# Optimization experiments

Hardware: AMD Instinct MI355X
Metric: run time of the kernel (lower is better)

Reference implementation:

```python
import jax, jax.numpy as jnp
import numpy as np

B, L, IN = 4, 2048, 64
D, N, K, NL, NC = 256, 16, 32, 2, 2


def _ln(x, g, b):
    m = x.mean(-1, keepdims=True)
    v = ((x - m) ** 2).mean(-1, keepdims=True)
    return (x - m) * jax.lax.rsqrt(v + 1e-5) * g + b


def _dwconv(x, w, b):
    # depthwise conv1d, kernel 3, padding 1; x: [B,L,D], w: [D,3]
    xp = jnp.pad(x, ((0, 0), (1, 1), (0, 0)))
    return xp[:, :-2] * w[:, 0] + xp[:, 1:-1] * w[:, 1] + xp[:, 2:] * w[:, 2] + b


def _ssm(x, loglam, wd, bd, wb, wc, wo, bo):
    # x: [B,L,D]
    lam = jax.nn.softplus(loglam)                      # [D,N]
    delta = jax.nn.softplus(x @ wd + bd)[..., None]    # [B,L,D,1]
    Bt = (x @ wb)[:, :, None, :]                       # [B,L,1,N]
    Ct = (x @ wc)[:, :, None, :]                       # [B,L,1,N]
    A_d = jnp.exp(-delta * lam)                        # [B,L,D,N]
    B_d = delta * Bt                                   # [B,L,D,N]
    A_l = jnp.moveaxis(A_d, 1, 0)                      # [L,B,D,N]
    B_l = jnp.moveaxis(B_d, 1, 0)

    def step(h, ab):
        a, b = ab
        h = a * h + b
        return h, h

    h0 = jnp.zeros((x.shape[0], D, N), x.dtype)
    _, hs = jax.lax.scan(step, h0, (A_l, B_l))         # [L,B,D,N]
    ys = hs * jnp.moveaxis(Ct, 1, 0)                   # [L,B,D,N]
    out = jnp.moveaxis(ys, 0, 1).reshape(x.shape[0], x.shape[1], D * N)
    return out @ wo + bo


def _temporal_block(x, lg, lb, cw, cb, loglam, wd, bd, wb, wc, wo, bo, gw, gb, pw, pb):
    res = x
    xn = _ln(x, lg, lb)
    xc = _dwconv(xn, cw, cb)
    xs = _ssm(xc, loglam, wd, bd, wb, wc, wo, bo)
    g = jax.nn.sigmoid(xn @ gw + gb)
    return (xs * g) @ pw + pb + res


def _spectral(x, fr, fi):
    X = jnp.fft.rfft(x, axis=1)                        # [B,F,D] complex64
    mag = jnp.abs(X).mean(axis=(0, 2))                 # [F]
    k = min(K, X.shape[1])
    _, idx = jax.lax.top_k(mag, k)
    filt = (fr[:, :k] + 1j * fi[:, :k]).T              # [k,D]
    Xk = X[:, idx, :] * filt[None]
    Xo = jnp.zeros(X.shape, X.dtype).at[:, idx, :].set(Xk)
    return jnp.fft.irfft(Xo, n=x.shape[1], axis=1)


def setup_inputs() -> dict:
    key = jax.random.key(0)
    ks = jax.random.split(key, 32)
    rn = lambda i, shape, s=0.02: jax.random.normal(ks[i], shape, jnp.float32) * s
    inp = {
        "x": jax.random.normal(ks[0], (B, L, IN), jnp.float32),
        "w_in": rn(1, (IN, D), 0.1), "b_in": jnp.zeros((D,), jnp.float32),
        "ln_g": jnp.ones((NL, D), jnp.float32), "ln_b": jnp.zeros((NL, D), jnp.float32),
        "conv_w": rn(2, (NL, D, 3), 0.3), "conv_b": jnp.zeros((NL, D), jnp.float32),
        "loglam": jax.random.uniform(ks[3], (NL, D, N), jnp.float32),
        "wd": rn(4, (NL, D, D), 0.05), "bd": jnp.zeros((NL, D), jnp.float32),
        "wb": rn(5, (NL, D, N), 0.05), "wc": rn(6, (NL, D, N), 0.05),
        "wo": rn(7, (NL, D * N, D), 0.01), "bo": jnp.zeros((NL, D), jnp.float32),
        "gate_w": rn(8, (NL, D, D), 0.05), "gate_b": jnp.zeros((NL, D), jnp.float32),
        "proj_w": rn(9, (NL, D, D), 0.05), "proj_b": jnp.zeros((NL, D), jnp.float32),
        "fr": rn(10, (D, K)), "fi": rn(11, (D, K)),
        "alpha": jnp.full((D,), 0.5, jnp.float32), "beta": jnp.full((D,), 0.5, jnp.float32),
        "g_out": jnp.ones((D,), jnp.float32), "b_out": jnp.zeros((D,), jnp.float32),
        "hw1": rn(12, (D, D // 2), 0.05), "hb1": jnp.zeros((D // 2,), jnp.float32),
        "hw2": rn(13, (D // 2, NC), 0.05), "hb2": jnp.zeros((NC,), jnp.float32),
    }
    return inp


def reference(x, w_in, b_in, ln_g, ln_b, conv_w, conv_b, loglam, wd, bd, wb, wc, wo, bo,
              gate_w, gate_b, proj_w, proj_b, fr, fi, alpha, beta, g_out, b_out,
              hw1, hb1, hw2, hb2):
    h = x @ w_in + b_in                                # [B,L,D]
    xt = h
    for i in range(NL):
        xt = _temporal_block(xt, ln_g[i], ln_b[i], conv_w[i], conv_b[i], loglam[i],
                             wd[i], bd[i], wb[i], wc[i], wo[i], bo[i],
                             gate_w[i], gate_b[i], proj_w[i], proj_b[i])
    xs = _spectral(h, fr, fi)
    z = alpha * xt + beta * xs
    z = _ln(z, g_out, b_out)
    zl = z[:, -1, :]                                   # [B,D]
    hid = jax.nn.silu(zl @ hw1 + hb1)                  # dropout is identity in eval
    return hid @ hw2 + hb2                             # [B,NC]
```

## Files before the change

### kernel.cpp

```cpp
#include <hip/hip_runtime.h>
#include <hip/hip_bf16.h>
#include <math.h>

#define BB   4
#define LL   2048
#define INF_ 64
#define DD   256
#define NN   16
#define KK   32
#define BLn  (BB*LL)
#define FCNT 1025
#define FSTR 1056
#define SKM  8192
#define SKN  256
#define PSZ  ((size_t)SKM * SKN)
#define IX(x) ((x) + ((x) >> 6))

typedef short short4v __attribute__((ext_vector_type(4)));
typedef short short8 __attribute__((ext_vector_type(8)));
typedef float f32x4  __attribute__((ext_vector_type(4)));

__device__ __forceinline__ float softplusf(float x) {
    return x > 20.f ? x : log1pf(__expf(x));
}
__device__ __forceinline__ float sigmoidf_(float x) {
    return 1.f / (1.f + __expf(-x));
}
__device__ __forceinline__ short bfs(float v) {
    __hip_bfloat16 h = __float2bfloat16(v);
    return *reinterpret_cast<short*>(&h);
}

__global__ void prep_kernel(const float* __restrict__ wd, const float* __restrict__ gw,
                            const float* __restrict__ pw, const float* __restrict__ wo,
                            const float* __restrict__ wb, const float* __restrict__ wc,
                            const float* __restrict__ w_in, float* __restrict__ tab,
                            __hip_bfloat16* __restrict__ cat0, __hip_bfloat16* __restrict__ cat1,
                            __hip_bfloat16* __restrict__ gwt, __hip_bfloat16* __restrict__ pwt,
                            __hip_bfloat16* __restrict__ wot, __hip_bfloat16* __restrict__ wint) {
    __shared__ float t[32][33];
    const int tid = threadIdx.x;
    int blk = blockIdx.x;
    if (blk < 8) {
        int i = blk * 256 + tid;
        if (i < 2048) {
            double ang = 2.0 * 3.14159265358979323846 * (double)i / 2048.0;
            tab[i]        = (float)cos(ang);
            tab[2048 + i] = (float)sin(ang);
        }
        return;
    }
    blk -= 8;
    const float* W; __hip_bfloat16* Wt; int K, N, bx, by;
    if (blk < 64)        { W = wd;                     Wt = cat0; K = 256;  N = 256; bx = blk & 7; by = blk >> 3; }
    else if (blk < 128)  { int q = blk - 64;  W = wd + 65536; Wt = cat1; K = 256; N = 256; bx = q & 7; by = q >> 3; }
    else if (blk < 192)  { int q = blk - 128; W = gw;  Wt = gwt;  K = 256;  N = 256; bx = q & 7; by = q >> 3; }
    else if (blk < 256)  { int q = blk - 192; W = pw;  Wt = pwt;  K = 256;  N = 256; bx = q & 7; by = q >> 3; }
    else if (blk < 1280) { int q = blk - 256; W = wo;  Wt = wot;  K = 4096; N = 256; bx = q & 7; by = q >> 3; }
    else if (blk < 1344) {
        int j = (blk - 1280) & 31;
        const float* src0 = (blk < 1312) ? wb : wb + DD * NN;
        const float* src1 = (blk < 1312) ? wc : wc + DD * NN;
        __hip_bfloat16* cat = (blk < 1312) ? cat0 : cat1;
        const float* src = (j < 16) ? src0 : src1;
        cat[(size_t)(256 + j) * 256 + tid] = __float2bfloat16(src[tid * 16 + (j & 15)]);
        return;
    } else { int q = blk - 1344; W = w_in; Wt = wint; K = 64; N = 256; bx = q & 7; by = q >> 3; }
    const int k0 = by * 32, n0 = bx * 32;
    if (k0 >= K) return;
    const int tx = tid & 31, ty = tid >> 5;
    for (int r = ty; r < 32; r += 8) t[r][tx] = W[(size_t)(k0 + r) * N + n0 + tx];
    __syncthreads();
    for (int r = ty; r < 32; r += 8)
        Wt[(size_t)(n0 + r) * K + k0 + tx] = __float2bfloat16(t[tx][r]);
}

__global__ __launch_bounds__(256)
void gemm_in_kernel(const float* __restrict__ x, const __hip_bfloat16* __restrict__ wint,
                    const float* __restrict__ b_in, float* __restrict__ h,
                    float* __restrict__ ht) {
    __shared__ alignas(16) short As[64][72];
    __shared__ alignas(16) short Bs[64][72];
    __shared__ float ts[64][68];
    const int tid = threadIdx.x;
    const int w = tid >> 6, lane = tid & 63;
    const int hi = lane >> 4, lo = lane & 15;
    const int row0 = blockIdx.y * 64, col0 = blockIdx.x * 64;
    const short* B = (const short*)wint;
#pragma unroll
    for (int e = 0; e < 4; ++e) {
        int q = e * 256 + tid;
        int r = q >> 4, c4 = (q & 15) * 4;
        float4 v = *(const float4*)&x[(size_t)(row0 + r) * 64 + c4];
        short4v s = {bfs(v.x), bfs(v.y), bfs(v.z), bfs(v.w)};
        *(short4v*)&As[r][c4] = s;
    }
#pragma unroll
    for (int e = 0; e < 2; ++e) {
        int q = e * 256 + tid;
        int r = q >> 3, c8 = (q & 7) * 8;
        *(short8*)&Bs[r][c8] = *(const short8*)&B[(size_t)(col0 + r) * 64 + c8];
    }
    __syncthreads();
    f32x4 acc[4];
    f32x4 zz = {0.f, 0.f, 0.f, 0.f};
#pragma unroll
    for (int n = 0; n < 4; ++n) acc[n] = zz;
#pragma unroll
    for (int s = 0; s < 2; ++s) {
        short8 af = *(const short8*)&As[w * 16 + lo][s * 32 + hi * 8];
#pragma unroll
        for (int n = 0; n < 4; ++n) {
            short8 bf = *(const short8*)&Bs[n * 16 + lo][s * 32 + hi * 8];
            acc[n] = __builtin_amdgcn_mfma_f32_16x16x32_bf16(af, bf, acc[n], 0, 0, 0);
        }
    }
#pragma unroll
    for (int n = 0; n < 4; ++n)
#pragma unroll
        for (int r = 0; r < 4; ++r) {
            const int row = row0 + w * 16 + hi * 4 + r;
            const int col = col0 + n * 16 + lo;
            float v = acc[n][r] + b_in[col];
            h[(size_t)row * 256 + col] = v;
            ts[n * 16 + lo][w * 16 + hi * 4 + r] = v;
        }
    __syncthreads();
    const int b = row0 >> 11, l0 = row0 & 2047, d0 = col0;
    const int dr = tid >> 2, seg = tid & 3;
    float* dst = ht + ((size_t)(b * 256 + d0 + dr)) * LL + l0 + seg * 16;
#pragma unroll
    for (int j = 0; j < 4; ++j)
        *(f32x4*)&dst[j * 4] = *(const f32x4*)&ts[dr][seg * 16 + j * 4];
}

__global__ __launch_bounds__(256)
void lnconv_kernel(const float* __restrict__ X, const float* __restrict__ g,
                   const float* __restrict__ bln, const float* __restrict__ cw,
                   const float* __restrict__ cb, __hip_bfloat16* __restrict__ xn_bf,
                   __hip_bfloat16* __restrict__ xc_bf) {
    __shared__ float xs[34][260];
    const int tid = threadIdx.x;
    const int w = tid >> 6, lane = tid & 63;
    const int blk = blockIdx.x;
    const int b = (blk * 32) >> 11, L0 = (blk * 32) & 2047;
    const float4 g4 = *(const float4*)&g[lane * 4];
    const float4 b4 = *(const float4*)&bln[lane * 4];
    for (int slot = w; slot < 34; slot += 4) {
        const int l = L0 - 1 + slot;
        if (l < 0 || l >= LL) {
            f32x4 z = {0.f, 0.f, 0.f, 0.f};
            *(f32x4*)&xs[slot][lane * 4] = z;
            continue;
        }
        float4 v = *(const float4*)&X[((size_t)b * LL + l) * DD + lane * 4];
        float s = v.x + v.y + v.z + v.w;
#pragma unroll
        for (int off = 1; off < 64; off <<= 1) s += __shfl_xor(s, off);
        float m = s * (1.f / DD);
        float cx = v.x - m, cy = v.y - m, cz = v.z - m, cw_ = v.w - m;
        float q = cx * cx + cy * cy + cz * cz + cw_ * cw_;
#pragma unroll
        for (int off = 1; off < 64; off <<= 1) q += __shfl_xor(q, off);
        float inv = rsqrtf(q * (1.f / DD) + 1e-5f);
        f32x4 y;
        y[0] = cx * inv * g4.x + b4.x;
        y[1] = cy * inv * g4.y + b4.y;
        y[2] = cz * inv * g4.z + b4.z;
        y[3] = cw_ * inv * g4.w + b4.w;
        *(f32x4*)&xs[slot][lane * 4] = y;
        if (slot >= 1 && slot <= 32) {
            short4v s4 = {bfs(y[0]), bfs(y[1]), bfs(y[2]), bfs(y[3])};
            *(short4v*)&xn_bf[((size_t)b * LL + l) * DD + lane * 4] = s4;
        }
    }
    __syncthreads();
    const int d = tid;
    const float w0 = cw[d * 3 + 0], w1 = cw[d * 3 + 1], w2 = cw[d * 3 + 2], cbd = cb[d];
    float xm = xs[0][d], x0 = xs[1][d];
    for (int rw = 0; rw < 32; ++rw) {
        float xp = xs[rw + 2][d];
        xc_bf[((size_t)b * LL + L0 + rw) * DD + d] =
            __float2bfloat16(fmaf(w0, xm, fmaf(w1, x0, fmaf(w2, xp, cbd))));
        xm = x0; x0 = xp;
    }
}

template<int MODE>
__global__ __launch_bounds__(256)
void gemm_core(const short* __restrict__ A, const short* __restrict__ Bw,
               const float* __restrict__ bias, const float* __restrict__ x1,
               const float* __restrict__ x2, float* __restrict__ o0,
               float* __restrict__ o1, float* __restrict__ o2,
               __hip_bfloat16* __restrict__ ob) {
    __shared__ alignas(16) short As[2][64][40];
    __shared__ alignas(16) short Bs[2][64][40];
    const int tid = threadIdx.x;
    const int w = tid >> 6, lane = tid & 63;
    const int hi = lane >> 4, lo = lane & 15;
    const int row0 = blockIdx.y * 64, col0 = blockIdx.x * 64;
    f32x4 acc[4];
    f32x4 zz = {0.f, 0.f, 0.f, 0.f};
#pragma unroll
    for (int n = 0; n < 4; ++n) acc[n] = zz;
    const int sr = tid >> 2, sc = (tid & 3) * 8;
    short8 pa = *(const short8*)&A[(size_t)(row0 + sr) * 256 + sc];
    short8 pb = *(const short8*)&Bw[(size_t)(col0 + sr) * 256 + sc];
    *(short8*)&As[0][sr][sc] = pa;
    *(short8*)&Bs[0][sr][sc] = pb;
    pa = *(const short8*)&A[(size_t)(row0 + sr) * 256 + 32 + sc];
    pb = *(const short8*)&Bw[(size_t)(col0 + sr) * 256 + 32 + sc];
    __syncthreads();
    int cur = 0;
    for (int it = 0; it < 8; ++it) {
        if (it + 1 < 8) {
            *(short8*)&As[cur ^ 1][sr][sc] = pa;
            *(short8*)&Bs[cur ^ 1][sr][sc] = pb;
        }
        if (it + 2 < 8) {
            const int k0 = (it + 2) << 5;
            pa = *(const short8*)&A[(size_t)(row0 + sr) * 256 + k0 + sc];
            pb = *(const short8*)&Bw[(size_t)(col0 + sr) * 256 + k0 + sc];
        }
        short8 af = *(const short8*)&As[cur][w * 16 + lo][hi * 8];
        short8 bfr[4];
#pragma unroll
        for (int n = 0; n < 4; ++n)
            bfr[n] = *(const short8*)&Bs[cur][n * 16 + lo][hi * 8];
#pragma unroll
        for (int n = 0; n < 4; ++n)
            acc[n] = __builtin_amdgcn_mfma_f32_16x16x32_bf16(af, bfr[n], acc[n], 0, 0, 0);
        __syncthreads();
        cur ^= 1;
    }
#pragma unroll
    for (int n = 0; n < 4; ++n) {
#pragma unroll
        for (int r = 0; r < 4; ++r) {
            const int row = row0 + w * 16 + hi * 4 + r;
            const int col = col0 + n * 16 + lo;
            float v = acc[n][r];
            if constexpr (MODE == 0) {
                if (col < 256)      o0[(size_t)row * 256 + col] = softplusf(v + bias[col]);
                else if (col < 272) o1[(size_t)row * 16 + col - 256] = v;
                else if (col < 288) o2[(size_t)row * 16 + col - 272] = v;
            } else if constexpr (MODE == 1) {
                float gv = sigmoidf_(v + bias[col]);
                size_t idx = (size_t)row * 256 + col;
                float s = x1[idx] + x1[PSZ + idx] + x2[col];
                ob[idx] = __float2bfloat16(gv * s);
            } else {
                o0[(size_t)row * 256 + col] = v + bias[col] + x1[(size_t)row * 256 + col];
            }
        }
    }
}

__global__ __launch_bounds__(256)
void gemm_sk_kernel(const __hip_bfloat16* __restrict__ Abf, const __hip_bfloat16* __restrict__ Wt,
                    float* __restrict__ P) {
    __shared__ alignas(16) short As[2][64][40];
    __shared__ alignas(16) short Bs[2][64][40];
    const int tid = threadIdx.x;
    const int f = blockIdx.x;
    const int xcd = f & 7, s = f >> 3;
    const int col = s & 3, u = s >> 2;
    const int rowkb = xcd + u * 8;
    const int row = rowkb & 127, kb = rowkb >> 7;
    const int row0 = row * 64, col0 = col * 64;
    const size_t kbase = (size_t)kb * 2048;
    const int w = tid >> 6, lane = tid & 63;
    const int hi = lane >> 4, lo = lane & 15;
    const short* A = (const short*)Abf;
    const short* B = (const short*)Wt;
    f32x4 acc[4];
    f32x4 zz = {0.f, 0.f, 0.f, 0.f};
#pragma unroll
    for (int n = 0; n < 4; ++n) acc[n] = zz;
    const int sr = tid >> 2, sc = (tid & 3) * 8;
    short8 pa = *(const short8*)&A[(size_t)(row0 + sr) * 4096 + kbase + sc];
    short8 pb = *(const short8*)&B[(size_t)(col0 + sr) * 4096 + kbase + sc];
    *(short8*)&As[0][sr][sc] = pa;
    *(short8*)&Bs[0][sr][sc] = pb;
    pa = *(const short8*)&A[(size_t)(row0 + sr) * 4096 + kbase + 32 + sc];
    pb = *(const short8*)&B[(size_t)(col0 + sr) * 4096 + kbase + 32 + sc];
    __syncthreads();
    int cur = 0;
    for (int it = 0; it < 64; ++it) {
        if (it + 1 < 64) {
            *(short8*)&As[cur ^ 1][sr][sc] = pa;
            *(short8*)&Bs[cur ^ 1][sr][sc] = pb;
        }
        if (it + 2 < 64) {
            const size_t k0 = kbase + ((it + 2) << 5);
            pa = *(const short8*)&A[(size_t)(row0 + sr) * 4096 + k0 + sc];
            pb = *(const short8*)&B[(size_t)(col0 + sr) * 4096 + k0 + sc];
        }
        short8 af = *(const short8*)&As[cur][w * 16 + lo][hi * 8];
        short8 bfr[4];
#pragma unroll
        for (int n = 0; n < 4; ++n)
            bfr[n] = *(const short8*)&Bs[cur][n * 16 + lo][hi * 8];
#pragma unroll
        for (int n = 0; n < 4; ++n)
            acc[n] = __builtin_amdgcn_mfma_f32_16x16x32_bf16(af, bfr[n], acc[n], 0, 0, 0);
        __syncthreads();
        cur ^= 1;
    }
    float* Pk = P + (size_t)kb * PSZ;
#pragma unroll
    for (int n = 0; n < 4; ++n)
#pragma unroll
        for (int r = 0; r < 4; ++r) {
            int rr = row0 + w * 16 + hi * 4 + r;
            int cc = col0 + n * 16 + lo;
            Pk[(size_t)rr * SKN + cc] = acc[n][r];
        }
}

template<int PHASE>
__global__ void ssm_chunk_kernel(const float* __restrict__ delta, const float* __restrict__ Bt,
                                 const float* __restrict__ Ct, const float* __restrict__ loglam,
                                 float* __restrict__ sA, float* __restrict__ sB,
                                 __hip_bfloat16* __restrict__ ys) {
    __shared__ float dl[128][16];
    __shared__ float btl[128][16];
    __shared__ float ctl[128][16];
    const int dblk = blockIdx.x, c = blockIdx.y, b = blockIdx.z;
    const int tid = threadIdx.x;
    const size_t lbase = (size_t)b * LL + c * 128;
    for (int i = tid; i < 2048; i += 256) {
        int l = i >> 4, q = i & 15;
        dl[l][q]  = delta[(lbase + l) * DD + dblk * 16 + q];
        btl[l][q] = Bt[(lbase + l) * NN + q];
        if (PHASE == 1) ctl[l][q] = Ct[(lbase + l) * NN + q];
    }
    float hv = 0.f, ap = 1.f;
    if (PHASE == 1) {
        for (int cc = 0; cc < c; ++cc) {
            size_t oi = ((size_t)(b * 16 + cc)) * 4096 + dblk * 256 + tid;
            hv = fmaf(sA[oi], hv, sB[oi]);
        }
    }
    __syncthreads();
    const int dloc = tid >> 4, n = tid & 15;
    const float lam = softplusf(loglam[(dblk * 16 + dloc) * NN + n]);
    for (int l = 0; l < 128; ++l) {
        float dv = dl[l][dloc];
        float a = __expf(-dv * lam);
        hv = fmaf(a, hv, dv * btl[l][n]);
        if (PHASE == 0) ap *= a;
        else ys[(lbase + l) * (DD * NN) + dblk * 256 + tid] = __float2bfloat16(hv * ctl[l][n]);
    }
    if (PHASE == 0) {
        size_t oi = ((size_t)(b * 16 + c)) * 4096 + dblk * 256 + tid;
        sA[oi] = ap; sB[oi] = hv;
    }
}

__global__ void last_ssm_part_kernel(const float* __restrict__ sA, const float* __restrict__ sB,
                                     const float* __restrict__ Ct,
                                     const float* __restrict__ wo, float* __restrict__ part) {
    __shared__ float hC[4][128];
    const int c = blockIdx.x, tid = threadIdx.x;
    const int p0 = c * 128;
#pragma unroll
    for (int e = 0; e < 2; ++e) {
        int i = e * 256 + tid;
        int b = i >> 7, p = i & 127;
        float hh = 0.f;
#pragma unroll
        for (int cc = 0; cc < 16; ++cc) {
            size_t oi = ((size_t)(b * 16 + cc)) * 4096 + p0 + p;
            hh = fmaf(sA[oi], hh, sB[oi]);
        }
        hC[b][p] = hh * Ct[((size_t)b * LL + (LL - 1)) * NN + (p & 15)];
    }
    __syncthreads();
    float a0 = 0.f, a1 = 0.f, a2 = 0.f, a3 = 0.f;
    for (int p = 0; p < 128; ++p) {
        float wv = wo[(size_t)(p0 + p) * DD + tid];
        a0 = fmaf(hC[0][p], wv, a0);
        a1 = fmaf(hC[1][p], wv, a1);
        a2 = fmaf(hC[2][p], wv, a2);
        a3 = fmaf(hC[3][p], wv, a3);
    }
    part[(0 * 32 + c) * DD + tid] = a0;
    part[(1 * 32 + c) * DD + tid] = a1;
    part[(2 * 32 + c) * DD + tid] = a2;
    part[(3 * 32 + c) * DD + tid] = a3;
}

__global__ void last_redproj_kernel(const float* __restrict__ part, const float* __restrict__ bo,
                                    const __hip_bfloat16* __restrict__ xn, const float* __restrict__ gw,
                                    const float* __restrict__ gb, const float* __restrict__ pw,
                                    const float* __restrict__ pb, const float* __restrict__ resid,
                                    float* __restrict__ xtlast) {
    __shared__ float xrow[256];
    __shared__ float xsg[256];
    const int b = blockIdx.x, d = threadIdx.x;
    float ol = bo[d];
#pragma unroll
    for (int c = 0; c < 32; ++c) ol += part[(b * 32 + c) * DD + d];
    const size_t rbase = ((size_t)b * LL + (LL - 1)) * DD;
    xrow[d] = __bfloat162float(xn[rbase + d]);
    __syncthreads();
    float acc = gb[d];
    for (int k = 0; k < 256; ++k) acc = fmaf(xrow[k], gw[(size_t)k * DD + d], acc);
    xsg[d] = ol * sigmoidf_(acc);
    __syncthreads();
    float acc2 = pb[d];
    for (int k = 0; k < 256; ++k) acc2 = fmaf(xsg[k], pw[(size_t)k * DD + d], acc2);
    xtlast[b * DD + d] = acc2 + resid[rbase + d];
}

__global__ __launch_bounds__(256)
void fft2_kernel(const float* __restrict__ ht, const float* __restrict__ tab,
                 float* __restrict__ Xre, float* __restrict__ Xim) {
    __shared__ float re[2080];
    __shared__ float im[2080];
    __shared__ float c2[2048];
    __shared__ float s2[2048];
    const int tid = threadIdx.x;
    const int pair = blockIdx.x;
    const int b = pair >> 7, d0 = pair & 127;
    for (int p = tid; p < 2048; p += 256) {
        if (p >= 1) {
            int lh = 31 - __clz((unsigned)p);
            int j = p - (1 << lh);
            int t = j << (10 - lh);
            c2[p] = tab[t]; s2[p] = tab[2048 + t];
        }
    }
    const float* ha = ht + ((size_t)b * 256 + d0) * LL;
    const float* hb = ha + (size_t)128 * LL;
    for (int i = tid; i < 2048; i += 256) {
        int r = (int)(__brev((unsigned)i) >> 21);
        re[IX(r)] = ha[i];
        im[IX(r)] = hb[i];
    }
    __syncthreads();
#pragma unroll
    for (int s = 1; s <= 11; ++s) {
        const int half = 1 << (s - 1);
#pragma unroll
        for (int e = 0; e < 4; ++e) {
            int q = e * 256 + tid;
            int j = q & (half - 1);
            int i0 = ((q >> (s - 1)) << s) + j;
            int i1 = i0 + half;
            float wr = c2[half + j], wi = -s2[half + j];
            float xr = re[IX(i1)], xi = im[IX(i1)];
            float tr = xr * wr - xi * wi;
            float ti = xr * wi + xi * wr;
            float ur = re[IX(i0)], ui = im[IX(i0)];
            re[IX(i0)] = ur + tr; im[IX(i0)] = ui + ti;
            re[IX(i1)] = ur - tr; im[IX(i1)] = ui - ti;
        }
        __syncthreads();
    }
    const int seqa = b * 256 + d0;
    float* xra = Xre + (size_t)seqa * FSTR;
    float* xia = Xim + (size_t)seqa * FSTR;
    float* xrb = xra + (size_t)128 * FSTR;
    float* xib = xia + (size_t)128 * FSTR;
    for (int f = tid; f < FCNT; f += 256) {
        int nf = (2048 - f) & 2047;
        float zrf = re[IX(f)], zif = im[IX(f)];
        float zrn = re[IX(nf)], zin = im[IX(nf)];
        xra[f] = 0.5f * (zrf + zrn);
        xia[f] = 0.5f * (zif - zin);
        xrb[f] = 0.5f * (zif + zin);
        xib[f] = 0.5f * (zrn - zrf);
    }
}

__global__ void mag_part_kernel(const float* __restrict__ Xre, const float* __restrict__ Xim,
                                float* __restrict__ part) {
    const int fb = blockIdx.x, sb = blockIdx.y;
    const int tid = threadIdx.x;
    const int f = fb * 256 + tid;
    float s = 0.f;
    if (f < FCNT) {
        for (int q = 0; q < 64; ++q) {
            size_t base = (size_t)(sb * 64 + q) * FSTR + f;
            float re = Xre[base], im = Xim[base];
            s += sqrtf(re * re + im * im);
        }
    }
    part[sb * 1280 + fb * 256 + tid] = s;
}

__global__ void topk_kernel(const float* __restrict__ part, int* __restrict__ sel) {
    __shared__ float vals[1280];
    __shared__ float wval[4][32];
    __shared__ int   widx[4][32];
    const int tid = threadIdx.x;
    const int lane = tid & 63, wid = tid >> 6;
    for (int i = tid; i < 1280; i += 256) {
        float v = -1e30f;
        if (i < FCNT) {
            v = 0.f;
#pragma unroll
            for (int sb = 0; sb < 16; ++sb) v += part[sb * 1280 + i];
        }
        vals[i] = v;
    }
    __syncthreads();
    const int base = wid * 320;
    for (int k = 0; k < 32; ++k) {
        float bv = -1e30f; int bi = 0x7fffffff;
#pragma unroll
        for (int q = 0; q < 5; ++q) {
            int i = base + q * 64 + lane;
            float v = vals[i];
            if (v > bv) { bv = v; bi = i; }
        }
#pragma unroll
        for (int off = 32; off > 0; off >>= 1) {
            float ov = __shfl_down(bv, off);
            int   oi = __shfl_down(bi, off);
            if (ov > bv || (ov == bv && oi < bi)) { bv = ov; bi = oi; }
        }
        bv = __shfl(bv, 0);
        bi = __shfl(bi, 0);
        if (lane == 0) { wval[wid][k] = bv; widx[wid][k] = bi; }
        vals[bi] = -1e30f;
    }
    __syncthreads();
    if (tid == 0) {
        int p0 = 0, p1 = 0, p2 = 0, p3 = 0;
        for (int k = 0; k < 32; ++k) {
            float v0 = wval[0][p0], v1 = wval[1][p1], v2 = wval[2][p2], v3 = wval[3][p3];
            int bw = 0; float bv = v0;
            if (v1 > bv) { bv = v1; bw = 1; }
            if (v2 > bv) { bv = v2; bw = 2; }
            if (v3 > bv) { bv = v3; bw = 3; }
            if (bw == 0)      { sel[k] = widx[0][p0++]; }
            else if (bw == 1) { sel[k] = widx[1][p1++]; }
            else if (bw == 2) { sel[k] = widx[2][p2++]; }
            else              { sel[k] = widx[3][p3++]; }
        }
    }
}

__global__ void head_kernel(const float* __restrict__ Xre, const float* __restrict__ Xim,
                            const int* __restrict__ sel, const float* __restrict__ fr,
                            const float* __restrict__ fi, const float* __restrict__ tab,
                            const float* __restrict__ xtlast,
                            const float* __restrict__ alpha, const float* __restrict__ beta,
                            const float* __restrict__ gout, const float* __restrict__ bout,
                            const float* __restrict__ hw1, const float* __restrict__ hb1,
                            const float* __restrict__ hw2, const float* __restrict__ hb2,
                            float* __restrict__ out) {
    __shared__ float red[256];
    __shared__ float z[256];
    __shared__ float hid[128];
    const int b = blockIdx.x, tid = threadIdx.x;
    const size_t sbase = (size_t)(b * 256 + tid) * FSTR;
    float xsl = 0.f;
    for (int j = 0; j < 32; ++j) {
        int f = sel[j];
        float xr = Xre[sbase + f];
        float xi = Xim[sbase + f];
        float frv = fr[tid * KK + j], fiv = fi[tid * KK + j];
        float xor_ = xr * frv - xi * fiv;
        float xoi  = xr * fiv + xi * frv;
        int kk2 = (f * (LL - 1)) & (LL - 1);
        float c = tab[kk2], s = tab[2048 + kk2];
        float w = (f == 0 || f == 1024) ? 1.f : 2.f;
        xsl = fmaf(w, xor_ * c - xoi * s, xsl);
    }
    xsl *= (1.f / LL);
    float zv = alpha[tid] * xtlast[b * 256 + tid] + beta[tid] * xsl;
    red[tid] = zv; __syncthreads();
    for (int s = 128; s > 0; s >>= 1) { if (tid < s) red[tid] += red[tid + s]; __syncthreads(); }
    float m = red[0] * (1.f / DD);
    __syncthreads();
    float c = zv - m;
    red[tid] = c * c; __syncthreads();
    for (int s = 128; s > 0; s >>= 1) { if (tid < s) red[tid] += red[tid + s]; __syncthreads(); }
    float var = red[0] * (1.f / DD);
    z[tid] = c * rsqrtf(var + 1e-5f) * gout[tid] + bout[tid];
    __syncthreads();
    if (tid < 128) {
        float a = hb1[tid];
        for (int k = 0; k < 256; ++k) a = fmaf(z[k], hw1[(size_t)k * 128 + tid], a);
        hid[tid] = a * sigmoidf_(a);
    }
    __syncthreads();
    if (tid < 2) {
        float a = hb2[tid];
        for (int k = 0; k < 128; ++k) a = fmaf(hid[k], hw2[(size_t)k * 2 + tid], a);
        out[b * 2 + tid] = a;
    }
}

extern "C" void kernel_launch(void* const* d_in, const int* in_sizes, int n_in,
                              void* d_out, int out_size, void* d_ws, size_t ws_size,
                              hipStream_t stream) {
    const float* x      = (const float*)d_in[0];
    const float* w_in   = (const float*)d_in[1];
    const float* b_in   = (const float*)d_in[2];
    const float* ln_g   = (const float*)d_in[3];
    const float* ln_b   = (const float*)d_in[4];
    const float* conv_w = (const float*)d_in[5];
    const float* conv_b = (const float*)d_in[6];
    const float* loglam = (const float*)d_in[7];
    const float* wd     = (const float*)d_in[8];
    const float* bd     = (const float*)d_in[9];
    const float* wb     = (const float*)d_in[10];
    const float* wc     = (const float*)d_in[11];
    const float* wo     = (const float*)d_in[12];
    const float* bo     = (const float*)d_in[13];
    const float* gw     = (const float*)d_in[14];
    const float* gb     = (const float*)d_in[15];
    const float* pw     = (const float*)d_in[16];
    const float* pb     = (const float*)d_in[17];
    const float* fr     = (const float*)d_in[18];
    const float* fi     = (const float*)d_in[19];
    const float* alpha  = (const float*)d_in[20];
    const float* beta   = (const float*)d_in[21];
    const float* gout   = (const float*)d_in[22];
    const float* bout   = (const float*)d_in[23];
    const float* hw1    = (const float*)d_in[24];
    const float* hb1    = (const float*)d_in[25];
    const float* hw2    = (const float*)d_in[26];
    const float* hb2    = (const float*)d_in[27];

    float* ws = (float*)d_ws;
    size_t o = 0;
    auto alloc = [&](size_t n) { float* p = ws + o; o += (n + 15) & ~(size_t)15; return p; };

    const size_t BLnDD = (size_t)BLn * DD;
    float* h      = alloc(BLnDD);
    float* xt1    = alloc(BLnDD);
    float* ht     = alloc(BLnDD);
    float* delta  = alloc(BLnDD);
    float* Pbuf   = alloc(2 * PSZ);
    float* Btm    = alloc((size_t)BLn * NN);
    float* Ctm    = alloc((size_t)BLn * NN);
    float* tab    = alloc(4096);
    float* ysf    = alloc(BLnDD * NN / 2);
    float* sA     = alloc((size_t)BB * 16 * 4096);
    float* sB     = alloc((size_t)BB * 16 * 4096);
    float* xnbf_f = alloc(BLnDD / 2);
    float* xcbf_f = alloc(BLnDD / 2);
    float* xsgf   = alloc(BLnDD / 2);
    float* cat0_f = alloc((size_t)320 * 256 / 2);
    float* cat1_f = alloc((size_t)320 * 256 / 2);
    float* gwt_f  = alloc((size_t)DD * DD / 2);
    float* pwt_f  = alloc((size_t)DD * DD / 2);
    float* wot_f  = alloc((size_t)DD * NN * DD / 2);
    float* wint_f = alloc((size_t)DD * 64 / 2);
    float* magp   = alloc(16 * 1280);
    int*   sel    = (int*)alloc(32);
    float* lpart  = alloc((size_t)BB * 32 * DD);
    float* xtlast = alloc(BB * DD);

    __hip_bfloat16* ys    = (__hip_bfloat16*)ysf;
    float*          Xre   = ysf;
    float*          Xim   = ysf + (size_t)1024 * FSTR;
    __hip_bfloat16* xn_bf = (__hip_bfloat16*)xnbf_f;
    __hip_bfloat16* xc_bf = (__hip_bfloat16*)xcbf_f;
    __hip_bfloat16* xsg_bf= (__hip_bfloat16*)xsgf;
    __hip_bfloat16* cat0  = (__hip_bfloat16*)cat0_f;
    __hip_bfloat16* cat1  = (__hip_bfloat16*)cat1_f;
    __hip_bfloat16* gwt   = (__hip_bfloat16*)gwt_f;
    __hip_bfloat16* pwt   = (__hip_bfloat16*)pwt_f;
    __hip_bfloat16* wot   = (__hip_bfloat16*)wot_f;
    __hip_bfloat16* wint  = (__hip_bfloat16*)wint_f;

    const dim3 blk(256);

    prep_kernel<<<1368, blk, 0, stream>>>(wd, gw, pw, wo, wb, wc, w_in, tab,
                                          cat0, cat1, gwt, pwt, wot, wint);
    gemm_in_kernel<<<dim3(4, 128), blk, 0, stream>>>(x, wint, b_in, h, ht);

    const dim3 qgrid(5, BLn / 64);
    const dim3 ggrid(4, BLn / 64);
    const dim3 sgrid(16, 16, BB);

    lnconv_kernel<<<BLn / 32, blk, 0, stream>>>(h, ln_g, ln_b, conv_w, conv_b, xn_bf, xc_bf);
    gemm_core<0><<<qgrid, blk, 0, stream>>>((const short*)xc_bf, (const short*)cat0,
                                            bd, nullptr, nullptr, delta, Btm, Ctm, nullptr);
    ssm_chunk_kernel<0><<<sgrid, blk, 0, stream>>>(delta, Btm, nullptr, loglam,
                                                   sA, sB, nullptr);
    ssm_chunk_kernel<1><<<sgrid, blk, 0, stream>>>(delta, Btm, Ctm, loglam,
                                                   sA, sB, ys);
    gemm_sk_kernel<<<1024, blk, 0, stream>>>(ys, wot, Pbuf);
    gemm_core<1><<<ggrid, blk, 0, stream>>>((const short*)xn_bf, (const short*)gwt,
                                            gb, Pbuf, bo, nullptr, nullptr, nullptr, xsg_bf);
    gemm_core<2><<<ggrid, blk, 0, stream>>>((const short*)xsg_bf, (const short*)pwt,
                                            pb, h, nullptr, xt1, nullptr, nullptr, nullptr);

    lnconv_kernel<<<BLn / 32, blk, 0, stream>>>(xt1, ln_g + DD, ln_b + DD,
                                                conv_w + DD * 3, conv_b + DD, xn_bf, xc_bf);
    gemm_core<0><<<qgrid, blk, 0, stream>>>((const short*)xc_bf, (const short*)cat1,
                                            bd + DD, nullptr, nullptr, delta, Btm, Ctm, nullptr);
    ssm_chunk_kernel<0><<<sgrid, blk, 0, stream>>>(delta, Btm, nullptr, loglam + DD * NN,
                                                   sA, sB, nullptr);
    last_ssm_part_kernel<<<32, blk, 0, stream>>>(sA, sB, Ctm, wo + (size_t)DD * NN * DD, lpart);
    last_redproj_kernel<<<BB, blk, 0, stream>>>(lpart, bo + DD, xn_bf,
                                                gw + (size_t)DD * DD, gb + DD,
                                                pw + (size_t)DD * DD, pb + DD, xt1, xtlast);

    fft2_kernel<<<512, blk, 0, stream>>>(ht, tab, Xre, Xim);
    mag_part_kernel<<<dim3(5, 16), blk, 0, stream>>>(Xre, Xim, magp);
    topk_kernel<<<1, blk, 0, stream>>>(magp, sel);

    head_kernel<<<BB, blk, 0, stream>>>(Xre, Xim, sel, fr, fi, tab, xtlast,
                                        alpha, beta, gout, bout,
                                        hw1, hb1, hw2, hb2, (float*)d_out);
}
```

Measured before the change: 280.2 us.

## Enlarge split-K GEMM tile to 128 rows and restructure double-buffered pipeline

The split-K output-projection GEMM now computes 128x64 tiles per block, with each wave doing two M sub-tiles, so every B fragment loaded from shared memory feeds two MFMAs. This halves the block count and cuts B-operand reloads. Both GEMM kernels also get a manually unrolled two-stage register/LDS pipeline that uses a raw barrier with an lgkmcnt wait instead of __syncthreads. The changes add register and LDS pressure, and with fewer blocks there may be less parallelism to hide latency.

```diff
diff --git a/kernel.cpp b/kernel.cpp
--- a/kernel.cpp
+++ b/kernel.cpp
@@ -30,6 +30,8 @@
     __hip_bfloat16 h = __float2bfloat16(v);
     return *reinterpret_cast<short*>(&h);
 }
+#define RAWBAR() do { asm volatile("s_waitcnt lgkmcnt(0)" ::: "memory"); \
+                      __builtin_amdgcn_s_barrier(); } while (0)
 
 __global__ void prep_kernel(const float* __restrict__ wd, const float* __restrict__ gw,
                             const float* __restrict__ pw, const float* __restrict__ wo,
@@ -204,34 +206,38 @@
 #pragma unroll
     for (int n = 0; n < 4; ++n) acc[n] = zz;
     const int sr = tid >> 2, sc = (tid & 3) * 8;
-    short8 pa = *(const short8*)&A[(size_t)(row0 + sr) * 256 + sc];
-    short8 pb = *(const short8*)&Bw[(size_t)(col0 + sr) * 256 + sc];
-    *(short8*)&As[0][sr][sc] = pa;
-    *(short8*)&Bs[0][sr][sc] = pb;
-    pa = *(const short8*)&A[(size_t)(row0 + sr) * 256 + 32 + sc];
-    pb = *(const short8*)&Bw[(size_t)(col0 + sr) * 256 + 32 + sc];
-    __syncthreads();
-    int cur = 0;
-    for (int it = 0; it < 8; ++it) {
-        if (it + 1 < 8) {
-            *(short8*)&As[cur ^ 1][sr][sc] = pa;
-            *(short8*)&Bs[cur ^ 1][sr][sc] = pb;
-        }
-        if (it + 2 < 8) {
-            const int k0 = (it + 2) << 5;
-            pa = *(const short8*)&A[(size_t)(row0 + sr) * 256 + k0 + sc];
-            pb = *(const short8*)&Bw[(size_t)(col0 + sr) * 256 + k0 + sc];
-        }
-        short8 af = *(const short8*)&As[cur][w * 16 + lo][hi * 8];
-        short8 bfr[4];
-#pragma unroll
-        for (int n = 0; n < 4; ++n)
-            bfr[n] = *(const short8*)&Bs[cur][n * 16 + lo][hi * 8];
-#pragma unroll
-        for (int n = 0; n < 4; ++n)
-            acc[n] = __builtin_amdgcn_mfma_f32_16x16x32_bf16(af, bfr[n], acc[n], 0, 0, 0);
-        __syncthreads();
-        cur ^= 1;
+    const size_t aoff = (size_t)(row0 + sr) * 256 + sc;
+    const size_t boff = (size_t)(col0 + sr) * 256 + sc;
+    short8 a_s0, b_s0, a_s1, b_s1;
+#define GC_LOAD0(t) { a_s0 = *(const short8*)&A[aoff + (t) * 32]; \
+                      b_s0 = *(const short8*)&Bw[boff + (t) * 32]; }
+#define GC_LOAD1(t) { a_s1 = *(const short8*)&A[aoff + (t) * 32]; \
+                      b_s1 = *(const short8*)&Bw[boff + (t) * 32]; }
+#define GC_WRITE0(buf) { *(short8*)&As[buf][sr][sc] = a_s0; *(short8*)&Bs[buf][sr][sc] = b_s0; }
+#define GC_WRITE1(buf) { *(short8*)&As[buf][sr][sc] = a_s1; *(short8*)&Bs[buf][sr][sc] = b_s1; }
+#define GC_COMPUTE(buf) { \
+        short8 af = *(const short8*)&As[buf][w * 16 + lo][hi * 8]; \
+        short8 bf0 = *(const short8*)&Bs[buf][0 * 16 + lo][hi * 8]; \
+        short8 bf1 = *(const short8*)&Bs[buf][1 * 16 + lo][hi * 8]; \
+        short8 bf2 = *(const short8*)&Bs[buf][2 * 16 + lo][hi * 8]; \
+        short8 bf3 = *(const short8*)&Bs[buf][3 * 16 + lo][hi * 8]; \
+        acc[0] = __builtin_amdgcn_mfma_f32_16x16x32_bf16(af, bf0, acc[0], 0, 0, 0); \
+        acc[1] = __builtin_amdgcn_mfma_f32_16x16x32_bf16(af, bf1, acc[1], 0, 0, 0); \
+        acc[2] = __builtin_amdgcn_mfma_f32_16x16x32_bf16(af, bf2, acc[2], 0, 0, 0); \
+        acc[3] = __builtin_amdgcn_mfma_f32_16x16x32_bf16(af, bf3, acc[3], 0, 0, 0); }
+    GC_LOAD0(0); GC_LOAD1(1);
+    GC_WRITE0(0);
+    RAWBAR();
+#pragma unroll
+    for (int j = 0; j < 8; j += 2) {
+        if (j + 2 < 8) GC_LOAD0(j + 2);
+        GC_WRITE1(1);
+        GC_COMPUTE(0);
+        RAWBAR();
+        if (j + 3 < 8) GC_LOAD1(j + 3);
+        if (j + 2 < 8) GC_WRITE0(0);
+        GC_COMPUTE(1);
+        RAWBAR();
     }
 #pragma unroll
     for (int n = 0; n < 4; ++n) {
@@ -259,63 +265,83 @@
 __global__ __launch_bounds__(256)
 void gemm_sk_kernel(const __hip_bfloat16* __restrict__ Abf, const __hip_bfloat16* __restrict__ Wt,
                     float* __restrict__ P) {
-    __shared__ alignas(16) short As[2][64][40];
+    __shared__ alignas(16) short As[2][128][40];
     __shared__ alignas(16) short Bs[2][64][40];
     const int tid = threadIdx.x;
     const int f = blockIdx.x;
-    const int xcd = f & 7, s = f >> 3;
-    const int col = s & 3, u = s >> 2;
-    const int rowkb = xcd + u * 8;
-    const int row = rowkb & 127, kb = rowkb >> 7;
-    const int row0 = row * 64, col0 = col * 64;
+    const int xcd = f & 7, slot = f >> 3;
+    const int col = slot & 3;
+    const int rk = xcd + (slot >> 2) * 8;
+    const int row = rk & 63, kb = rk >> 6;
+    const int row0 = row * 128, col0 = col * 64;
     const size_t kbase = (size_t)kb * 2048;
     const int w = tid >> 6, lane = tid & 63;
     const int hi = lane >> 4, lo = lane & 15;
     const short* A = (const short*)Abf;
     const short* B = (const short*)Wt;
-    f32x4 acc[4];
+    f32x4 acc[2][4];
     f32x4 zz = {0.f, 0.f, 0.f, 0.f};
 #pragma unroll
-    for (int n = 0; n < 4; ++n) acc[n] = zz;
-    const int sr = tid >> 2, sc = (tid & 3) * 8;
-    short8 pa = *(const short8*)&A[(size_t)(row0 + sr) * 4096 + kbase + sc];
-    short8 pb = *(const short8*)&B[(size_t)(col0 + sr) * 4096 + kbase + sc];
-    *(short8*)&As[0][sr][sc] = pa;
-    *(short8*)&Bs[0][sr][sc] = pb;
-    pa = *(const short8*)&A[(size_t)(row0 + sr) * 4096 + kbase + 32 + sc];
-    pb = *(const short8*)&B[(size_t)(col0 + sr) * 4096 + kbase + 32 + sc];
-    __syncthreads();
-    int cur = 0;
-    for (int it = 0; it < 64; ++it) {
-        if (it + 1 < 64) {
-            *(short8*)&As[cur ^ 1][sr][sc] = pa;
-            *(short8*)&Bs[cur ^ 1][sr][sc] = pb;
-        }
-        if (it + 2 < 64) {
-            const size_t k0 = kbase + ((it + 2) << 5);
-            pa = *(const short8*)&A[(size_t)(row0 + sr) * 4096 + k0 + sc];
-            pb = *(const short8*)&B[(size_t)(col0 + sr) * 4096 + k0 + sc];
-        }
-        short8 af = *(const short8*)&As[cur][w * 16 + lo][hi * 8];
-        short8 bfr[4];
+    for (int m = 0; m < 2; ++m)
+#pragma unroll
+        for (int n = 0; n < 4; ++n) acc[m][n] = zz;
+    const int ra0 = tid >> 2,          ca0 = (tid & 3) * 8;
+    const int ra1 = (256 + tid) >> 2,  ca1 = ((256 + tid) & 3) * 8;
+    const size_t aoff0 = (size_t)(row0 + ra0) * 4096 + kbase + ca0;
+    const size_t aoff1 = (size_t)(row0 + ra1) * 4096 + kbase + ca1;
+    const size_t boff  = (size_t)(col0 + ra0) * 4096 + kbase + ca0;
+    short8 a0_s0, a1_s0, b_s0, a0_s1, a1_s1, b_s1;
+#define SK_LOAD0(t) { size_t k0 = (size_t)(t) * 32; \
+        a0_s0 = *(const short8*)&A[aoff0 + k0]; \
+        a1_s0 = *(const short8*)&A[aoff1 + k0]; \
+        b_s0  = *(const short8*)&B[boff  + k0]; }
+#define SK_LOAD1(t) { size_t k0 = (size_t)(t) * 32; \
+        a0_s1 = *(const short8*)&A[aoff0 + k0]; \
+        a1_s1 = *(const short8*)&A[aoff1 + k0]; \
+        b_s1  = *(const short8*)&B[boff  + k0]; }
+#define SK_WRITE0(buf) { *(short8*)&As[buf][ra0][ca0] = a0_s0; \
+        *(short8*)&As[buf][ra1][ca1] = a1_s0; *(short8*)&Bs[buf][ra0][ca0] = b_s0; }
+#define SK_WRITE1(buf) { *(short8*)&As[buf][ra0][ca0] = a0_s1; \
+        *(short8*)&As[buf][ra1][ca1] = a1_s1; *(short8*)&Bs[buf][ra0][ca0] = b_s1; }
+#define SK_COMPUTE(buf) { \
+        short8 af0 = *(const short8*)&As[buf][w * 32 + 0 * 16 + lo][hi * 8]; \
+        short8 af1 = *(const short8*)&As[buf][w * 32 + 1 * 16 + lo][hi * 8]; \
+        short8 bf0 = *(const short8*)&Bs[buf][0 * 16 + lo][hi * 8]; \
+        short8 bf1 = *(const short8*)&Bs[buf][1 * 16 + lo][hi * 8]; \
+        short8 bf2 = *(const short8*)&Bs[buf][2 * 16 + lo][hi * 8]; \
+        short8 bf3 = *(const short8*)&Bs[buf][3 * 16 + lo][hi * 8]; \
+        acc[0][0] = __builtin_amdgcn_mfma_f32_16x16x32_bf16(af0, bf0, acc[0][0], 0, 0, 0); \
+        acc[0][1] = __builtin_amdgcn_mfma_f32_16x16x32_bf16(af0, bf1, acc[0][1], 0, 0, 0); \
+        acc[0][2] = __builtin_amdgcn_mfma_f32_16x16x32_bf16(af0, bf2, acc[0][2], 0, 0, 0); \
+        acc[0][3] = __builtin_amdgcn_mfma_f32_16x16x32_bf16(af0, bf3, acc[0][3], 0, 0, 0); \
+        acc[1][0] = __builtin_amdgcn_mfma_f32_16x16x32_bf16(af1, bf0, acc[1][0], 0, 0, 0); \
+        acc[1][1] = __builtin_amdgcn_mfma_f32_16x16x32_bf16(af1, bf1, acc[1][1], 0, 0, 0); \
+        acc[1][2] = __builtin_amdgcn_mfma_f32_16x16x32_bf16(af1, bf2, acc[1][2], 0, 0, 0); \
+        acc[1][3] = __builtin_amdgcn_mfma_f32_16x16x32_bf16(af1, bf3, acc[1][3], 0, 0, 0); }
+    SK_LOAD0(0); SK_LOAD1(1);
+    SK_WRITE0(0);
+    RAWBAR();
+    for (int j = 0; j < 64; j += 2) {
+        if (j + 2 < 64) SK_LOAD0(j + 2);
+        SK_WRITE1(1);
+        SK_COMPUTE(0);
+        RAWBAR();
+        if (j + 3 < 64) SK_LOAD1(j + 3);
+        if (j + 2 < 64) SK_WRITE0(0);
+        SK_COMPUTE(1);
+        RAWBAR();
+    }
+    float* Pk = P + (size_t)kb * PSZ;
+#pragma unroll
+    for (int m = 0; m < 2; ++m)
 #pragma unroll
         for (int n = 0; n < 4; ++n)
-            bfr[n] = *(const short8*)&Bs[cur][n * 16 + lo][hi * 8];
-#pragma unroll
-        for (int n = 0; n < 4; ++n)
-            acc[n] = __builtin_amdgcn_mfma_f32_16x16x32_bf16(af, bfr[n], acc[n], 0, 0, 0);
-        __syncthreads();
-        cur ^= 1;
-    }
-    float* Pk = P + (size_t)kb * PSZ;
-#pragma unroll
-    for (int n = 0; n < 4; ++n)
-#pragma unroll
-        for (int r = 0; r < 4; ++r) {
-            int rr = row0 + w * 16 + hi * 4 + r;
-            int cc = col0 + n * 16 + lo;
-            Pk[(size_t)rr * SKN + cc] = acc[n][r];
-        }
+#pragma unroll
+            for (int r = 0; r < 4; ++r) {
+                int rr = row0 + w * 32 + m * 16 + hi * 4 + r;
+                int cc = col0 + n * 16 + lo;
+                Pk[(size_t)rr * SKN + cc] = acc[m][n][r];
+            }
 }
 
 template<int PHASE>
@@ -688,7 +714,7 @@
                                                    sA, sB, nullptr);
     ssm_chunk_kernel<1><<<sgrid, blk, 0, stream>>>(delta, Btm, Ctm, loglam,
                                                    sA, sB, ys);
-    gemm_sk_kernel<<<1024, blk, 0, stream>>>(ys, wot, Pbuf);
+    gemm_sk_kernel<<<512, blk, 0, stream>>>(ys, wot, Pbuf);
     gemm_core<1><<<ggrid, blk, 0, stream>>>((const short*)xn_bf, (const short*)gwt,
                                             gb, Pbuf, bo, nullptr, nullptr, nullptr, xsg_bf);
     gemm_core<2><<<ggrid, blk, 0, stream>>>((const short*)xsg_bf, (const short*)pwt,
```

After: 279.3 us. About the same (-0.3%).
